# Kernel tuning notes

Measured on AMD Instinct MI355X. Metric: run time of the kernel, lower is better.

Reference implementation:

```python
import jax, jax.numpy as jnp
import numpy as np

DIM = 1024
HEADS = 16
HEAD_DIM = DIM // HEADS
THRESH = 0.29514
SHARP = 15.0
LN_EPS = 1e-5
NORM_EPS = 1e-12


def setup_inputs() -> dict:
    key = jax.random.key(0)
    ks = jax.random.split(key, 8)
    s = 1.0 / np.sqrt(DIM)
    sg = 1.0 / np.sqrt(HEAD_DIM)
    return {
        "x": jax.random.normal(ks[0], (2, 2048, DIM), dtype=jnp.float32),
        "Wq": jax.random.uniform(ks[1], (DIM, DIM), jnp.float32, -s, s),
        "Wk": jax.random.uniform(ks[2], (DIM, DIM), jnp.float32, -s, s),
        "Wv": jax.random.uniform(ks[3], (DIM, DIM), jnp.float32, -s, s),
        "gq": jax.random.uniform(ks[4], (HEAD_DIM,), jnp.float32, -sg, sg),
        "gk": jax.random.uniform(ks[5], (HEAD_DIM,), jnp.float32, -sg, sg),
        "Wo": jax.random.uniform(ks[6], (DIM, DIM), jnp.float32, -s, s),
        "bo": jax.random.uniform(ks[7], (DIM,), jnp.float32, -s, s),
        "ln_w": jnp.ones((DIM,), jnp.float32),
        "ln_b": jnp.zeros((DIM,), jnp.float32),
    }


def _l2norm(t):
    # F.normalize: t / max(||t||_2, eps)
    n = jnp.sqrt(jnp.sum(t * t, axis=-1, keepdims=True))
    return t / jnp.maximum(n, NORM_EPS)


def reference(x, Wq, Wk, Wv, gq, gk, Wo, bo, ln_w, ln_b):
    B, T, D = x.shape
    # LayerNorm over last dim
    mu = jnp.mean(x, axis=-1, keepdims=True)
    var = jnp.mean((x - mu) ** 2, axis=-1, keepdims=True)
    x_norm = (x - mu) / jnp.sqrt(var + LN_EPS) * ln_w + ln_b

    def split_heads(t):  # [B,T,D] -> [B,H,T,hd]
        return t.reshape(B, T, HEADS, HEAD_DIM).transpose(0, 2, 1, 3)

    q = _l2norm(split_heads(x_norm @ Wq))
    k = _l2norm(split_heads(x_norm @ Wk))
    v = split_heads(x @ Wv)  # note: v uses un-normalized x, as in source

    align = jnp.einsum("bhtd,bhsd->bhts", q, k)  # cosine alignment
    resonance = jax.nn.sigmoid((align - THRESH) * SHARP)
    gate_q = jnp.einsum("bhtd,d->bht", q, gq)
    gate_k = jnp.einsum("bhsd,d->bhs", k, gk)
    modulation = resonance * gate_q[..., :, None] * gate_k[..., None, :]
    collapse = jnp.einsum("bhts,bhsd->bhtd", modulation, v)
    collapse = collapse.transpose(0, 2, 1, 3).reshape(B, T, D)
    return collapse @ Wo + bo
```

## Files before the change

### kernel.cpp

```cpp
#include <hip/hip_runtime.h>
#include <math.h>

#define DIM 1024
#define T_SEQ 2048
#define NBATCH 2
#define HEADS 16
#define HD 64
#define NTOK 4096
#define THRESH 0.29514f
#define SHARP 15.0f
#define LOG2E 1.4426950408889634f

typedef __attribute__((ext_vector_type(8))) short bf16x8;
typedef __attribute__((ext_vector_type(4))) float f32x4;
typedef __attribute__((ext_vector_type(4))) unsigned int u32x4;

__device__ __forceinline__ unsigned short f2b(float f) {
    unsigned int u = __float_as_uint(f);
    unsigned int r = (u + 0x7FFFu + ((u >> 16) & 1u)) >> 16;
    return (unsigned short)r;
}
__device__ __forceinline__ float b2f(unsigned short u) {
    return __uint_as_float(((unsigned int)u) << 16);
}
__device__ __forceinline__ unsigned int pack2_bf16(float lo, float hi) {
    unsigned int a = __float_as_uint(lo) + 0x8000u;
    unsigned int b = __float_as_uint(hi) + 0x8000u;
    return __builtin_amdgcn_perm(b, a, 0x07060302u);
}

__device__ __forceinline__ void async_cp16(const unsigned short* g, unsigned short* l) {
    __builtin_amdgcn_global_load_lds(
        (const __attribute__((address_space(1))) unsigned int*)g,
        (__attribute__((address_space(3))) unsigned int*)l, 16, 0, 0);
}

__global__ __launch_bounds__(256) void ln_xnorm_kernel(
    const float* __restrict__ x, const float* __restrict__ lnw, const float* __restrict__ lnb,
    unsigned short* __restrict__ xnb, unsigned short* __restrict__ xb) {
    int row = blockIdx.x * 4 + (threadIdx.x >> 6);
    int lane = threadIdx.x & 63;
    const float4* xr = (const float4*)(x + (size_t)row * DIM);
    float4 v[4];
    float s = 0.f, ss = 0.f;
#pragma unroll
    for (int i = 0; i < 4; i++) {
        v[i] = xr[lane + i * 64];
        s += v[i].x + v[i].y + v[i].z + v[i].w;
        ss += v[i].x * v[i].x + v[i].y * v[i].y + v[i].z * v[i].z + v[i].w * v[i].w;
    }
#pragma unroll
    for (int off = 32; off; off >>= 1) {
        s += __shfl_xor(s, off);
        ss += __shfl_xor(ss, off);
    }
    float m = s * (1.f / DIM);
    float rstd = rsqrtf(ss * (1.f / DIM) - m * m + 1e-5f);
#pragma unroll
    for (int i = 0; i < 4; i++) {
        int e = (lane + i * 64) * 4;
        float4 lw = *(const float4*)&lnw[e];
        float4 lb = *(const float4*)&lnb[e];
        ushort4 un, ur;
        un.x = f2b((v[i].x - m) * rstd * lw.x + lb.x);
        un.y = f2b((v[i].y - m) * rstd * lw.y + lb.y);
        un.z = f2b((v[i].z - m) * rstd * lw.z + lb.z);
        un.w = f2b((v[i].w - m) * rstd * lw.w + lb.w);
        ur.x = f2b(v[i].x); ur.y = f2b(v[i].y); ur.z = f2b(v[i].z); ur.w = f2b(v[i].w);
        *(ushort4*)&xnb[(size_t)row * DIM + e] = un;
        *(ushort4*)&xb[(size_t)row * DIM + e] = ur;
    }
}

__global__ __launch_bounds__(256) void wtrans_kernel(
    const float* __restrict__ W0, const float* __restrict__ W1,
    const float* __restrict__ W2, const float* __restrict__ W3,
    unsigned short* __restrict__ T0, unsigned short* __restrict__ T1,
    unsigned short* __restrict__ T2, unsigned short* __restrict__ T3) {
    __shared__ float tile[64][65];
    const int z = blockIdx.z;
    const float* W = (z == 0) ? W0 : (z == 1) ? W1 : (z == 2) ? W2 : W3;
    unsigned short* T = (z == 0) ? T0 : (z == 1) ? T1 : (z == 2) ? T2 : T3;
    const int k0 = blockIdx.x * 64, n0 = blockIdx.y * 64;
    const int r = threadIdx.x >> 3;
    const int c = (threadIdx.x & 7) * 8;
#pragma unroll
    for (int half = 0; half < 2; half++) {
        int rr = r + half * 32;
        float4 a = *(const float4*)&W[(size_t)(k0 + rr) * DIM + n0 + c];
        float4 b = *(const float4*)&W[(size_t)(k0 + rr) * DIM + n0 + c + 4];
        tile[rr][c + 0] = a.x; tile[rr][c + 1] = a.y; tile[rr][c + 2] = a.z; tile[rr][c + 3] = a.w;
        tile[rr][c + 4] = b.x; tile[rr][c + 5] = b.y; tile[rr][c + 6] = b.z; tile[rr][c + 7] = b.w;
    }
    __syncthreads();
#pragma unroll
    for (int half = 0; half < 2; half++) {
        int dd = r + half * 32;
        bf16x8 o;
#pragma unroll
        for (int j = 0; j < 8; j++) o[j] = (short)f2b(tile[c + j][dd]);
        *(bf16x8*)&T[(size_t)(n0 + dd) * DIM + k0 + c] = o;
    }
}

template <int MODE>
__global__ __launch_bounds__(256) void gemm_mfma_kernel(
    const unsigned short* __restrict__ A0, const unsigned short* __restrict__ A2,
    const unsigned short* __restrict__ Bt0, const unsigned short* __restrict__ Bt1,
    const unsigned short* __restrict__ Bt2, const float* __restrict__ bias,
    const float* __restrict__ gq, const float* __restrict__ gk,
    unsigned short* __restrict__ Oq, unsigned short* __restrict__ Ok,
    unsigned short* __restrict__ Ov, float* __restrict__ gq_t, float* __restrict__ gk_t,
    float* __restrict__ Oout) {
    __shared__ __align__(16) unsigned short As[128 * 32];
    __shared__ __align__(16) unsigned short Bs[128 * 32];
    const int tid = threadIdx.x;
    const int lane = tid & 63, w = tid >> 6;
    const int l16 = lane & 15, quad = lane >> 4;
    const int wm = w >> 1, wn = w & 1;
    const int m0 = blockIdx.x * 128, n0 = blockIdx.y * 128;
    const unsigned short* A;
    const unsigned short* Bt;
    int z = 0;
    if constexpr (MODE == 0) {
        z = blockIdx.z;
        A = (z == 2) ? A2 : A0;
        Bt = (z == 0) ? Bt0 : (z == 1) ? Bt1 : Bt2;
    } else {
        A = A0;
        Bt = Bt0;
    }
    f32x4 acc[4][4] = {};
    const int kswz = (l16 >> 1) & 3;

    for (int k0 = 0; k0 < DIM; k0 += 32) {
        __syncthreads();
#pragma unroll
        for (int i = 0; i < 2; i++) {
            int linear = i * 256 + tid;
            int m = linear >> 2, kgp = linear & 3;
            int kgl = kgp ^ ((m >> 1) & 3);
            async_cp16(A + (size_t)(m0 + m) * DIM + k0 + kgl * 8, As + linear * 8);
            async_cp16(Bt + (size_t)(n0 + m) * DIM + k0 + kgl * 8, Bs + linear * 8);
        }
        __syncthreads();
        bf16x8 af[4], bfr[4];
#pragma unroll
        for (int t = 0; t < 4; t++) {
            int ma = wm * 64 + t * 16 + l16;
            af[t] = *(const bf16x8*)(As + ma * 32 + ((quad ^ kswz) * 8));
            int nb = wn * 64 + t * 16 + l16;
            bfr[t] = *(const bf16x8*)(Bs + nb * 32 + ((quad ^ kswz) * 8));
        }
#pragma unroll
        for (int mt = 0; mt < 4; mt++)
#pragma unroll
            for (int nt = 0; nt < 4; nt++)
                acc[mt][nt] =
                    __builtin_amdgcn_mfma_f32_16x16x32_bf16(af[mt], bfr[nt], acc[mt][nt], 0, 0, 0);
    }

    if constexpr (MODE == 0) {
        const int h = (n0 + wn * 64) >> 6;
        if (z <= 1) {
            constexpr float QSCALE = -SHARP * LOG2E;
            const float* gvec = (z == 0) ? gq : gk;
            float* gate = (z == 0) ? gq_t : gk_t;
            unsigned short* O = (z == 0) ? Oq : Ok;
            const float oscale = (z == 0) ? QSCALE : 1.0f;
            float gv[4];
#pragma unroll
            for (int nt = 0; nt < 4; nt++) gv[nt] = gvec[nt * 16 + l16];
#pragma unroll
            for (int mt = 0; mt < 4; mt++) {
#pragma unroll
                for (int r = 0; r < 4; r++) {
                    float ss = 0.f;
#pragma unroll
                    for (int nt = 0; nt < 4; nt++) ss += acc[mt][nt][r] * acc[mt][nt][r];
#pragma unroll
                    for (int msk = 1; msk < 16; msk <<= 1) ss += __shfl_xor(ss, msk);
                    float rn = __builtin_amdgcn_rcpf(fmaxf(sqrtf(ss), 1e-12f));
                    float vn[4], gg = 0.f;
#pragma unroll
                    for (int nt = 0; nt < 4; nt++) {
                        vn[nt] = acc[mt][nt][r] * rn;
                        gg += vn[nt] * gv[nt];
                    }
#pragma unroll
                    for (int msk = 1; msk < 16; msk <<= 1) gg += __shfl_xor(gg, msk);
                    int tok = m0 + wm * 64 + mt * 16 + quad * 4 + r;
                    int b = tok >> 11, t = tok & 2047;
                    size_t rowbase = ((size_t)(b * HEADS + h) * T_SEQ + t) * HD;
#pragma unroll
                    for (int nt = 0; nt < 4; nt++)
                        O[rowbase + nt * 16 + l16] = f2b(vn[nt] * oscale);
                    if (l16 == 0) gate[(b * HEADS + h) * T_SEQ + t] = gg;
                }
            }
        } else {
#pragma unroll
            for (int mt = 0; mt < 4; mt++) {
#pragma unroll
                for (int r = 0; r < 4; r++) {
                    int tok = m0 + wm * 64 + mt * 16 + quad * 4 + r;
                    int b = tok >> 11, t = tok & 2047;
                    size_t rowbase = ((size_t)(b * HEADS + h) * T_SEQ + t) * HD;
#pragma unroll
                    for (int nt = 0; nt < 4; nt++)
                        Ov[rowbase + nt * 16 + l16] = f2b(acc[mt][nt][r]);
                }
            }
        }
    } else {
        float bias_r[4];
#pragma unroll
        for (int nt = 0; nt < 4; nt++) bias_r[nt] = bias[n0 + wn * 64 + nt * 16 + l16];
#pragma unroll
        for (int mt = 0; mt < 4; mt++) {
#pragma unroll
            for (int r = 0; r < 4; r++) {
                int tok = m0 + wm * 64 + mt * 16 + quad * 4 + r;
#pragma unroll
                for (int nt = 0; nt < 4; nt++) {
                    int n = n0 + wn * 64 + nt * 16 + l16;
                    Oout[(size_t)tok * DIM + n] = acc[mt][nt][r] + bias_r[nt];
                }
            }
        }
    }
}

__global__ __launch_bounds__(256) void vtrans_kernel(const unsigned short* __restrict__ Vn,
                                                     const float* __restrict__ gk_t,
                                                     unsigned short* __restrict__ Vt) {
    __shared__ float tile[64][65];
    const int bh = blockIdx.y;
    const int t0 = blockIdx.x * 64;
    const int r = threadIdx.x >> 3;
    const int c = (threadIdx.x & 7) * 8;
    const unsigned short* src = Vn + (size_t)bh * T_SEQ * HD;
#pragma unroll
    for (int half = 0; half < 2; half++) {
        int rr = r + half * 32;
        float gkv = gk_t[bh * T_SEQ + t0 + rr];
        bf16x8 v = *(const bf16x8*)(src + (size_t)(t0 + rr) * HD + c);
#pragma unroll
        for (int j = 0; j < 8; j++) tile[rr][c + j] = b2f((unsigned short)v[j]) * gkv;
    }
    __syncthreads();
    unsigned short* dst = Vt + (size_t)bh * HD * T_SEQ;
#pragma unroll
    for (int half = 0; half < 2; half++) {
        int dd = r + half * 32;
        bf16x8 o;
#pragma unroll
        for (int j = 0; j < 8; j++) o[j] = (short)f2b(tile[c + j][dd]);
        *(bf16x8*)(dst + (size_t)dd * T_SEQ + t0 + c) = o;
    }
}

__global__ __launch_bounds__(256, 4) void attn_mfma_kernel(
    const unsigned short* __restrict__ Qn, const unsigned short* __restrict__ Kn,
    const unsigned short* __restrict__ Vt, const float* __restrict__ gateq,
    unsigned short* __restrict__ collp0, unsigned short* __restrict__ collp1) {
    __shared__ __align__(16) unsigned short Ks[2][64 * 64];
    __shared__ __align__(16) unsigned short VtL[2][64 * 64];
    const int tid = threadIdx.x;
    const int lane = tid & 63, w = tid >> 6;
    const int quad = lane >> 4, l16 = lane & 15;
    const int f = blockIdx.x + 16 * blockIdx.y + 256 * blockIdx.z;
    const int q_ = f >> 3;
    const int panel = (f & 7) * 8 + (q_ >> 4);
    const int t0 = (q_ & 15) * 128;
    const int h = panel & 15;
    const int zz = panel >> 4;
    const int b = zz >> 1, shalf = zz & 1;
    const int sbase = shalf * (T_SEQ / 2);
    const int bh = b * HEADS + h;
    const size_t base = (size_t)bh * T_SEQ * HD;
    constexpr float K0 = THRESH * SHARP * LOG2E;
    const f32x4 k0v = {K0, K0, K0, K0};

    int det0 = quad, det1 = quad + 4;
    asm("v_permlane16_swap_b32 %0, %1" : "+v"(det0), "+v"(det1));
    const bool flagA = (__builtin_amdgcn_readfirstlane(det0) == 0);

    bf16x8 fq[2][2];
#pragma unroll
    for (int mt = 0; mt < 2; mt++) {
        const unsigned short* qrow = Qn + base + (size_t)(t0 + w * 32 + mt * 16 + l16) * HD;
        fq[mt][0] = *(const bf16x8*)(qrow + quad * 8);
        fq[mt][1] = *(const bf16x8*)(qrow + 32 + quad * 8);
    }

    f32x4 oacc[4][2] = {};
    const int srow = tid >> 3;
    const int sgp = tid & 7;
    const int swz = l16 & 7;

    auto stage_chunk = [&](unsigned short* ksn, unsigned short* vtn, int s0) {
#pragma unroll
        for (int half = 0; half < 2; half++) {
            int row = srow + half * 32;
            int g = sgp ^ (row & 7);
            async_cp16(Kn + base + (size_t)(s0 + row) * HD + g * 8, ksn + row * 64 + sgp * 8);
            async_cp16(Vt + base + (size_t)row * T_SEQ + s0 + g * 8, vtn + row * 64 + sgp * 8);
        }
    };

    auto do_chunk = [&](const unsigned short* ksb, const unsigned short* vtb) {
#pragma unroll
        for (int kh = 0; kh < 2; kh++) {
            unsigned int p[2][2][2];
#pragma unroll
            for (int ct2 = 0; ct2 < 2; ct2++) {
                const int ct = 2 * kh + ct2;
                const unsigned short* krow = ksb + (ct * 16 + l16) * 64;
                bf16x8 fk0 = *(const bf16x8*)(krow + (quad ^ swz) * 8);
                bf16x8 fk1 = *(const bf16x8*)(krow + ((quad + 4) ^ swz) * 8);
#pragma unroll
                for (int mt = 0; mt < 2; mt++) {
                    __builtin_amdgcn_s_setprio(1);
                    f32x4 s1 =
                        __builtin_amdgcn_mfma_f32_16x16x32_bf16(fk0, fq[mt][0], k0v, 0, 0, 0);
                    f32x4 sacc =
                        __builtin_amdgcn_mfma_f32_16x16x32_bf16(fk1, fq[mt][1], s1, 0, 0, 0);
                    __builtin_amdgcn_s_setprio(0);
                    float w0 = __builtin_amdgcn_rcpf(1.f + __builtin_amdgcn_exp2f(sacc[0]));
                    float w1 = __builtin_amdgcn_rcpf(1.f + __builtin_amdgcn_exp2f(sacc[1]));
                    float w2 = __builtin_amdgcn_rcpf(1.f + __builtin_amdgcn_exp2f(sacc[2]));
                    float w3 = __builtin_amdgcn_rcpf(1.f + __builtin_amdgcn_exp2f(sacc[3]));
                    p[mt][ct2][0] = pack2_bf16(w0, w1);
                    p[mt][ct2][1] = pack2_bf16(w2, w3);
                }
            }
            int gv = (4 * kh + 2 * (quad & 1) + (quad >> 1)) ^ swz;
            bf16x8 fv[4];
#pragma unroll
            for (int dt = 0; dt < 4; dt++)
                fv[dt] = *(const bf16x8*)(vtb + (dt * 16 + l16) * 64 + gv * 8);
#pragma unroll
            for (int mt = 0; mt < 2; mt++) {
                unsigned int aL = p[mt][0][0], aH = p[mt][0][1];
                unsigned int bL = p[mt][1][0], bH = p[mt][1][1];
                asm("v_permlane16_swap_b32 %0, %1" : "+v"(aL), "+v"(bL));
                asm("v_permlane16_swap_b32 %0, %1" : "+v"(aH), "+v"(bH));
                u32x4 bt;
                if (flagA) {
                    bt.x = aL; bt.y = aH; bt.z = bL; bt.w = bH;
                } else {
                    bt.x = bL; bt.y = bH; bt.z = aL; bt.w = aH;
                }
                bf16x8 fs = __builtin_bit_cast(bf16x8, bt);
                __builtin_amdgcn_s_setprio(1);
#pragma unroll
                for (int dt = 0; dt < 4; dt++)
                    oacc[dt][mt] =
                        __builtin_amdgcn_mfma_f32_16x16x32_bf16(fv[dt], fs, oacc[dt][mt], 0, 0, 0);
                __builtin_amdgcn_s_setprio(0);
            }
        }
        __syncthreads();
    };

    stage_chunk(&Ks[0][0], &VtL[0][0], sbase);
    __syncthreads();

    for (int j = 0; j < T_SEQ / 256; j++) {
        stage_chunk(&Ks[1][0], &VtL[1][0], sbase + j * 128 + 64);
        do_chunk(&Ks[0][0], &VtL[0][0]);
        if (j + 1 < T_SEQ / 256) stage_chunk(&Ks[0][0], &VtL[0][0], sbase + j * 128 + 128);
        do_chunk(&Ks[1][0], &VtL[1][0]);
    }

    unsigned short* collp = shalf ? collp1 : collp0;
#pragma unroll
    for (int mt = 0; mt < 2; mt++) {
        int t = t0 + w * 32 + mt * 16 + l16;
        float gq_v = gateq[bh * T_SEQ + t];
        unsigned short* dst = collp + ((size_t)b * T_SEQ + t) * DIM + h * HD;
#pragma unroll
        for (int dt = 0; dt < 4; dt++) {
            ushort4 o;
            o.x = f2b(oacc[dt][mt][0] * gq_v);
            o.y = f2b(oacc[dt][mt][1] * gq_v);
            o.z = f2b(oacc[dt][mt][2] * gq_v);
            o.w = f2b(oacc[dt][mt][3] * gq_v);
            *(ushort4*)(dst + dt * 16 + quad * 4) = o;
        }
    }
}

__global__ __launch_bounds__(256) void merge_kernel(unsigned short* __restrict__ p0,
                                                    const unsigned short* __restrict__ p1) {
    size_t i = ((size_t)blockIdx.x * 256 + threadIdx.x) * 8;
    bf16x8 a = *(const bf16x8*)(p0 + i);
    bf16x8 c = *(const bf16x8*)(p1 + i);
    bf16x8 o;
#pragma unroll
    for (int j = 0; j < 8; j++)
        o[j] = (short)f2b(b2f((unsigned short)a[j]) + b2f((unsigned short)c[j]));
    *(bf16x8*)(p0 + i) = o;
}

extern "C" void kernel_launch(void* const* d_in, const int* in_sizes, int n_in,
                              void* d_out, int out_size, void* d_ws, size_t ws_size,
                              hipStream_t stream) {
    const float* x = (const float*)d_in[0];
    const float* Wq = (const float*)d_in[1];
    const float* Wk = (const float*)d_in[2];
    const float* Wv = (const float*)d_in[3];
    const float* gq = (const float*)d_in[4];
    const float* gk = (const float*)d_in[5];
    const float* Wo = (const float*)d_in[6];
    const float* bo = (const float*)d_in[7];
    const float* lnw = (const float*)d_in[8];
    const float* lnb = (const float*)d_in[9];
    float* out = (float*)d_out;

    unsigned short* ws = (unsigned short*)d_ws;
    unsigned short* xnb = ws;
    unsigned short* xb = xnb + (size_t)NTOK * DIM;
    unsigned short* Wqt = xb + (size_t)NTOK * DIM;
    unsigned short* Wkt = Wqt + (size_t)DIM * DIM;
    unsigned short* Wvt = Wkt + (size_t)DIM * DIM;
    unsigned short* Wot = Wvt + (size_t)DIM * DIM;
    unsigned short* Q16 = Wot + (size_t)DIM * DIM;
    unsigned short* K16 = Q16 + (size_t)NTOK * DIM;
    unsigned short* Vn = K16 + (size_t)NTOK * DIM;
    float* gq_t = (float*)(Vn + (size_t)NTOK * DIM);
    float* gk_t = gq_t + NBATCH * HEADS * T_SEQ;
    unsigned short* collb1 = (unsigned short*)(gk_t + NBATCH * HEADS * T_SEQ);
    unsigned short* Vt = xnb;
    unsigned short* collb0 = xb;

    ln_xnorm_kernel<<<NTOK / 4, 256, 0, stream>>>(x, lnw, lnb, xnb, xb);
    wtrans_kernel<<<dim3(16, 16, 4), 256, 0, stream>>>(Wq, Wk, Wv, Wo, Wqt, Wkt, Wvt, Wot);
    gemm_mfma_kernel<0><<<dim3(NTOK / 128, DIM / 128, 3), 256, 0, stream>>>(
        xnb, xb, Wqt, Wkt, Wvt, nullptr, gq, gk, Q16, K16, Vn, gq_t, gk_t, nullptr);
    vtrans_kernel<<<dim3(T_SEQ / 64, NBATCH * HEADS), 256, 0, stream>>>(Vn, gk_t, Vt);
    attn_mfma_kernel<<<dim3(T_SEQ / 128, HEADS, NBATCH * 2), 256, 0, stream>>>(
        Q16, K16, Vt, gq_t, collb0, collb1);
    merge_kernel<<<(NTOK * DIM) / (256 * 8), 256, 0, stream>>>(collb0, collb1);
    gemm_mfma_kernel<1><<<dim3(NTOK / 128, DIM / 128, 1), 256, 0, stream>>>(
        collb0, nullptr, Wot, nullptr, nullptr, bo, nullptr, nullptr, nullptr, nullptr, nullptr,
        nullptr, nullptr, out);
}
```

Measured before the change: 219.2 us.

## Double-buffer LDS tiles in MFMA GEMM to overlap loads with compute

The shared A/B tiles in the projection GEMM become two buffers. The next K-slice is prefetched asynchronously into the other buffer while MFMAs run on the current one. This replaces two barriers per K-step with a single barrier at the end of each iteration and hides global-load latency behind the matrix math. It doubles LDS use per block, which may lower occupancy, and it relies on the barrier also waiting for the outstanding async copies.

```diff
diff --git a/kernel.cpp b/kernel.cpp
--- a/kernel.cpp
+++ b/kernel.cpp
@@ -112,8 +112,8 @@
     unsigned short* __restrict__ Oq, unsigned short* __restrict__ Ok,
     unsigned short* __restrict__ Ov, float* __restrict__ gq_t, float* __restrict__ gk_t,
     float* __restrict__ Oout) {
-    __shared__ __align__(16) unsigned short As[128 * 32];
-    __shared__ __align__(16) unsigned short Bs[128 * 32];
+    __shared__ __align__(16) unsigned short As[2][128 * 32];
+    __shared__ __align__(16) unsigned short Bs[2][128 * 32];
     const int tid = threadIdx.x;
     const int lane = tid & 63, w = tid >> 6;
     const int l16 = lane & 15, quad = lane >> 4;
@@ -133,24 +133,30 @@
     f32x4 acc[4][4] = {};
     const int kswz = (l16 >> 1) & 3;
 
-    for (int k0 = 0; k0 < DIM; k0 += 32) {
-        __syncthreads();
-#pragma unroll
-        for (int i = 0; i < 2; i++) {
-            int linear = i * 256 + tid;
-            int m = linear >> 2, kgp = linear & 3;
-            int kgl = kgp ^ ((m >> 1) & 3);
-            async_cp16(A + (size_t)(m0 + m) * DIM + k0 + kgl * 8, As + linear * 8);
-            async_cp16(Bt + (size_t)(n0 + m) * DIM + k0 + kgl * 8, Bs + linear * 8);
-        }
-        __syncthreads();
+    const int lin0 = tid, lin1 = 256 + tid;
+    const int sm0 = lin0 >> 2, sk0 = (lin0 & 3) ^ ((sm0 >> 1) & 3);
+    const int sm1 = lin1 >> 2, sk1 = (lin1 & 3) ^ ((sm1 >> 1) & 3);
+
+    auto stage = [&](int kb, int k0) {
+        async_cp16(A + (size_t)(m0 + sm0) * DIM + k0 + sk0 * 8, &As[kb][lin0 * 8]);
+        async_cp16(Bt + (size_t)(n0 + sm0) * DIM + k0 + sk0 * 8, &Bs[kb][lin0 * 8]);
+        async_cp16(A + (size_t)(m0 + sm1) * DIM + k0 + sk1 * 8, &As[kb][lin1 * 8]);
+        async_cp16(Bt + (size_t)(n0 + sm1) * DIM + k0 + sk1 * 8, &Bs[kb][lin1 * 8]);
+    };
+
+    stage(0, 0);
+    __syncthreads();
+
+    for (int ks = 0; ks < DIM / 32; ks++) {
+        const int cur = ks & 1;
+        if (ks + 1 < DIM / 32) stage(cur ^ 1, (ks + 1) * 32);
         bf16x8 af[4], bfr[4];
 #pragma unroll
         for (int t = 0; t < 4; t++) {
             int ma = wm * 64 + t * 16 + l16;
-            af[t] = *(const bf16x8*)(As + ma * 32 + ((quad ^ kswz) * 8));
+            af[t] = *(const bf16x8*)(&As[cur][ma * 32 + ((quad ^ kswz) * 8)]);
             int nb = wn * 64 + t * 16 + l16;
-            bfr[t] = *(const bf16x8*)(Bs + nb * 32 + ((quad ^ kswz) * 8));
+            bfr[t] = *(const bf16x8*)(&Bs[cur][nb * 32 + ((quad ^ kswz) * 8)]);
         }
 #pragma unroll
         for (int mt = 0; mt < 4; mt++)
@@ -158,6 +164,7 @@
             for (int nt = 0; nt < 4; nt++)
                 acc[mt][nt] =
                     __builtin_amdgcn_mfma_f32_16x16x32_bf16(af[mt], bfr[nt], acc[mt][nt], 0, 0, 0);
+        __syncthreads();
     }
 
     if constexpr (MODE == 0) {
```

Result: no change. 216.4 us (-1.3%).
